# Kernel tuning notes

Hardware: AMD Instinct MI355X
Metric: run time of the kernel (lower is better)

The kernel has to match this reference:

```python
import jax, jax.numpy as jnp
import numpy as np

B, S, E, H = 2, 2048, 1024, 16
HD = E // H
SCALE = 1.0 / np.sqrt(HD)
PR_QKV = 0.05   # precision_ratio for q/k/v (critical_attention=False)
PR_OUT = 0.10
ROUTE_THR = 0.05  # gradient_threshold (critical_attention=False)
LN_EPS = 1e-5


def rpb_linear(x, W, b, precision_ratio):
    """ResidualPrecisionBoostLinear: ternary-quantized weight (threshold 0.7*mean|W|,
    per-tensor scale) plus top-`precision_ratio` fraction of residual kept full precision."""
    absW = jnp.abs(W)
    thr = 0.7 * jnp.mean(absW)
    tmask = (absW > thr).astype(W.dtype)
    scale = jnp.sum(absW * tmask) / jnp.maximum(jnp.sum(tmask), 1.0)
    Wq = scale * jnp.sign(W) * tmask
    res = W - Wq
    k = int(precision_ratio * W.size)
    kth = jax.lax.top_k(jnp.abs(res).ravel(), k)[0][-1]
    W_eff = Wq + res * (jnp.abs(res) >= kth).astype(W.dtype)
    return x @ W_eff.T + b


def selective_route(x, threshold):
    # forward: zero out small-magnitude activations (straight-through in training)
    return x * (jnp.abs(x) >= threshold).astype(x.dtype)


def layer_norm(x, g, b):
    mu = jnp.mean(x, axis=-1, keepdims=True)
    var = jnp.mean(jnp.square(x - mu), axis=-1, keepdims=True)
    return (x - mu) * jax.lax.rsqrt(var + LN_EPS) * g + b


def setup_inputs() -> dict:
    key = jax.random.key(0)
    ks = jax.random.split(key, 12)
    f = lambda k, shp, s=1.0: jax.random.normal(k, shp, dtype=jnp.float32) * s
    return {
        "query": f(ks[0], (B, S, E)),
        "key": f(ks[1], (B, S, E)),
        "value": f(ks[2], (B, S, E)),
        "Wq": f(ks[3], (E, E), 0.02), "bq": jnp.zeros((E,), jnp.float32),
        "Wk": f(ks[4], (E, E), 0.02), "bk": jnp.zeros((E,), jnp.float32),
        "Wv": f(ks[5], (E, E), 0.02), "bv": jnp.zeros((E,), jnp.float32),
        "Wo": f(ks[6], (E, E), 0.02), "bo": jnp.zeros((E,), jnp.float32),
        "ln_g": jnp.ones((E,), jnp.float32),
        "ln_b": jnp.zeros((E,), jnp.float32),
    }


def reference(query, key, value, Wq, bq, Wk, bk, Wv, bv, Wo, bo, ln_g, ln_b):
    qn = layer_norm(query, ln_g, ln_b)
    q = selective_route(rpb_linear(qn, Wq, bq, PR_QKV), ROUTE_THR)
    k = selective_route(rpb_linear(key, Wk, bk, PR_QKV), ROUTE_THR)
    v = selective_route(rpb_linear(value, Wv, bv, PR_QKV), ROUTE_THR)
    # [B,S,E] -> [B,H,S,HD]
    q = q.reshape(B, S, H, HD).transpose(0, 2, 1, 3)
    k = k.reshape(B, S, H, HD).transpose(0, 2, 1, 3)
    v = v.reshape(B, S, H, HD).transpose(0, 2, 1, 3)
    scores = jnp.einsum("bhqd,bhkd->bhqk", q, k) * SCALE
    attn = jax.nn.softmax(scores, axis=-1)   # dropout is identity in eval
    ctx = jnp.einsum("bhqk,bhkd->bhqd", attn, v)
    ctx = ctx.transpose(0, 2, 1, 3).reshape(B, S, E)
    return rpb_linear(ctx, Wo, bo, PR_OUT)
```

## Files before the change

### kernel.cpp

```cpp
#include <hip/hip_runtime.h>
#include <stdio.h>
#include <stdint.h>

#define BB 2
#define SS 2048
#define ED 1024
#define HH 16
#define HDD 64
#define MROWS 4096
#define NW_ELEM 1048576u

typedef unsigned short ushortT;
typedef __attribute__((ext_vector_type(8))) short bf16x8;
typedef __attribute__((ext_vector_type(4))) float f32x4;
typedef __attribute__((ext_vector_type(16))) float f32x16;

#define U_WHI 0u
#define U_WLO 4194304u
#define U_AH  8388608u
#define U_BH  12582912u
#define U_QH  16777216u
#define U_KH  20971520u
#define U_VH  25165824u
#define U_CH  29360128u
#define U_CL  33554432u
#define SMALL_OFF  75497472u
#define HIST_OFF   SMALL_OFF
#define ABS_OFF    (SMALL_OFF + 16384u)
#define MSK_OFF    (ABS_OFF + 32u)
#define CNT_OFF    (MSK_OFF + 32u)
#define SMALL_BYTES 16464u
#define WS_NEEDED  (SMALL_OFF + SMALL_BYTES)

#define SC44 17592186044416.0f
#define INV44 (1.0 / 17592186044416.0)

__device__ __forceinline__ const float* wsel(int w, const float* W0, const float* W1,
                                             const float* W2, const float* W3) {
  return w == 0 ? W0 : w == 1 ? W1 : w == 2 ? W2 : W3;
}

__device__ __forceinline__ ushortT f2bf(float x) {
  unsigned u = __float_as_uint(x);
  unsigned r = (u + 0x7FFFu + ((u >> 16) & 1u)) >> 16;
  return (ushortT)r;
}
__device__ __forceinline__ float bf2f(ushortT b) {
  return __uint_as_float(((unsigned)b) << 16);
}
__device__ __forceinline__ void bsplit(float x, ushortT& h, ushortT& l) {
  ushortT hb = f2bf(x);
  float hf = bf2f(hb);
  h = hb;
  l = f2bf(x - hf);
}
__device__ __forceinline__ unsigned pkbf(float a, float b) {
  unsigned r;
  asm("v_cvt_pk_bf16_f32 %0, %1, %2" : "=v"(r) : "v"(a), "v"(b));
  return r;
}
__device__ __forceinline__ void plswap(unsigned& a, unsigned& b) {
  asm("v_permlane32_swap_b32 %0, %1" : "+v"(a), "+v"(b));
}

__device__ __forceinline__ void gld_lds16(const ushortT* g, ushortT* s) {
  __builtin_amdgcn_global_load_lds((__attribute__((address_space(1))) void*)g,
                                   (__attribute__((address_space(3))) void*)s, 16, 0, 0);
}

__device__ __forceinline__ float get_thr(const unsigned long long* sAbs, int w) {
  return 0.7f * (float)((double)sAbs[w] * INV44 / 1048576.0);
}
__device__ __forceinline__ float get_scale(const unsigned long long* sMsk,
                                           const unsigned* cnt, int w) {
  double s = (double)sMsk[w] * INV44;
  return (float)s / fmaxf((float)cnt[w], 1.0f);
}

__device__ __forceinline__ void scan_sel(const unsigned* hist, unsigned& k, unsigned& prefix,
                                         unsigned* sh, int t) {
  sh[t] = hist[t];
  __syncthreads();
  for (int off = 1; off < 256; off <<= 1) {
    unsigned add = (t + off < 256) ? sh[t + off] : 0u;
    __syncthreads();
    sh[t] += add;
    __syncthreads();
  }
  int sel = __syncthreads_count((int)(sh[t] >= k)) - 1;
  unsigned suf = sh[sel];
  k -= (suf - hist[sel]);
  prefix = (prefix << 8) | (unsigned)sel;
  __syncthreads();
}

__global__ __launch_bounds__(256) void k_wstats(const float* W0, const float* W1,
                                                const float* W2, const float* W3,
                                                unsigned long long* sAbs) {
  const int w = blockIdx.y, t = threadIdx.x;
  const float* W = wsel(w, W0, W1, W2, W3) + blockIdx.x * 4096;
  unsigned long long s = 0;
#pragma unroll
  for (int r = 0; r < 4; r++) {
    float4 v = *(const float4*)(W + (t + 256 * r) * 4);
    s += (unsigned long long)(fabsf(v.x) * SC44);
    s += (unsigned long long)(fabsf(v.y) * SC44);
    s += (unsigned long long)(fabsf(v.z) * SC44);
    s += (unsigned long long)(fabsf(v.w) * SC44);
  }
  __shared__ unsigned long long sd[256];
  sd[t] = s;
  __syncthreads();
  for (int off = 128; off > 0; off >>= 1) {
    if (t < off) sd[t] += sd[t + off];
    __syncthreads();
  }
  if (!t) atomicAdd(&sAbs[w], sd[0]);
}

__global__ __launch_bounds__(256) void k_masked(const float* W0, const float* W1,
                                                const float* W2, const float* W3,
                                                const unsigned long long* sAbs,
                                                unsigned long long* sMsk, unsigned* sCnt) {
  const int w = blockIdx.y, t = threadIdx.x;
  const float thr = get_thr(sAbs, w);
  const float* W = wsel(w, W0, W1, W2, W3) + blockIdx.x * 4096;
  unsigned long long s = 0;
  unsigned c = 0;
#pragma unroll
  for (int r = 0; r < 4; r++) {
    float4 v = *(const float4*)(W + (t + 256 * r) * 4);
    float xs[4] = {v.x, v.y, v.z, v.w};
#pragma unroll
    for (int q = 0; q < 4; q++) {
      float a = fabsf(xs[q]);
      if (a > thr) { s += (unsigned long long)(a * SC44); c++; }
    }
  }
  __shared__ unsigned long long sd[256];
  __shared__ unsigned sc[256];
  sd[t] = s; sc[t] = c;
  __syncthreads();
  for (int off = 128; off > 0; off >>= 1) {
    if (t < off) { sd[t] += sd[t + off]; sc[t] += sc[t + off]; }
    __syncthreads();
  }
  if (!t) { atomicAdd(&sMsk[w], sd[0]); atomicAdd(&sCnt[w], sc[0]); }
}

__global__ __launch_bounds__(256) void k_hist(const float* W0, const float* W1,
                                              const float* W2, const float* W3,
                                              const unsigned long long* sAbs,
                                              const unsigned long long* sMsk,
                                              const unsigned* sCnt,
                                              unsigned* histG, int pass) {
  const int w = blockIdx.y, t = threadIdx.x;
  __shared__ unsigned sh[256];
  __shared__ unsigned h[256];
  const float thr = get_thr(sAbs, w);
  const float scale = get_scale(sMsk, sCnt, w);
  unsigned k = (w == 3) ? 104857u : 52428u, prefix = 0u;
  for (int pp = 0; pp < pass; pp++)
    scan_sel(histG + (pp * 4 + w) * 256, k, prefix, sh, t);

  h[t] = 0;
  __syncthreads();
  const float* W = wsel(w, W0, W1, W2, W3) + blockIdx.x * 4096;
  const int shift1 = 32 - 8 * pass;
  const int shift2 = 24 - 8 * pass;
#pragma unroll
  for (int r = 0; r < 4; r++) {
    float4 v = *(const float4*)(W + (t + 256 * r) * 4);
    float xs[4] = {v.x, v.y, v.z, v.w};
#pragma unroll
    for (int q = 0; q < 4; q++) {
      float x = xs[q];
      float a = fabsf(x);
      float wq = (a > thr) ? copysignf(scale, x) : 0.0f;
      unsigned bits = __float_as_uint(fabsf(x - wq));
      if (pass == 0) {
        atomicAdd(&h[bits >> 24], 1u);
      } else {
        if ((bits >> shift1) == prefix)
          atomicAdd(&h[(bits >> shift2) & 255u], 1u);
      }
    }
  }
  __syncthreads();
  if (h[t]) atomicAdd(&histG[(pass * 4 + w) * 256 + t], h[t]);
}

__global__ __launch_bounds__(256) void k_weff(const float* W0, const float* W1,
                                              const float* W2, const float* W3,
                                              const unsigned long long* sAbs,
                                              const unsigned long long* sMsk,
                                              const unsigned* sCnt,
                                              const unsigned* histG,
                                              ushortT* Whi, ushortT* Wlo) {
  const int w = blockIdx.y, t = threadIdx.x;
  __shared__ unsigned sh[256];
  const float thr = get_thr(sAbs, w);
  const float scale = get_scale(sMsk, sCnt, w);
  unsigned k = (w == 3) ? 104857u : 52428u, kth = 0u;
  for (int pp = 0; pp < 4; pp++)
    scan_sel(histG + (pp * 4 + w) * 256, k, kth, sh, t);

  const unsigned idx = (blockIdx.x * 256 + t) * 4;
  const float* W = wsel(w, W0, W1, W2, W3);
  float4 v = *(const float4*)(W + idx);
  float xs[4] = {v.x, v.y, v.z, v.w};
  ushort4 h4, l4;
#pragma unroll
  for (int c = 0; c < 4; c++) {
    float x = xs[c];
    float a = fabsf(x);
    float wq = (a > thr) ? copysignf(scale, x) : 0.0f;
    float res = x - wq;
    unsigned bits = __float_as_uint(fabsf(res));
    float we = wq + ((bits >= kth) ? res : 0.0f);
    ushortT hh, ll;
    bsplit(we, hh, ll);
    ((ushortT*)&h4)[c] = hh;
    ((ushortT*)&l4)[c] = ll;
  }
  *(ushort4*)&Whi[(size_t)w * NW_ELEM + idx] = h4;
  *(ushort4*)&Wlo[(size_t)w * NW_ELEM + idx] = l4;
}

__global__ __launch_bounds__(256) void k_pre(const float* __restrict__ query,
                                             const float* __restrict__ key,
                                             const float* __restrict__ g,
                                             const float* __restrict__ b,
                                             ushortT* __restrict__ Ah,
                                             ushortT* __restrict__ Bh) {
  const int t = threadIdx.x;
  if (blockIdx.y == 0) {
    const int row = blockIdx.x;
    __shared__ float red[8];
    float4 v = *(const float4*)&query[(size_t)row * ED + t * 4];
    float s = v.x + v.y + v.z + v.w;
#pragma unroll
    for (int m = 32; m; m >>= 1) s += __shfl_xor(s, m, 64);
    if ((t & 63) == 0) red[t >> 6] = s;
    __syncthreads();
    float mu = (red[0] + red[1] + red[2] + red[3]) * (1.0f / 1024.0f);
    float dx = v.x - mu, dy = v.y - mu, dz = v.z - mu, dw = v.w - mu;
    float s2 = dx * dx + dy * dy + dz * dz + dw * dw;
#pragma unroll
    for (int m = 32; m; m >>= 1) s2 += __shfl_xor(s2, m, 64);
    if ((t & 63) == 0) red[4 + (t >> 6)] = s2;
    __syncthreads();
    float var = (red[4] + red[5] + red[6] + red[7]) * (1.0f / 1024.0f);
    float inv = rsqrtf(var + 1e-5f);
    float4 gg = *(const float4*)&g[t * 4];
    float4 bb = *(const float4*)&b[t * 4];
    float ys[4] = {dx * inv * gg.x + bb.x, dy * inv * gg.y + bb.y,
                   dz * inv * gg.z + bb.z, dw * inv * gg.w + bb.w};
    ushort4 h4;
#pragma unroll
    for (int c = 0; c < 4; c++) ((ushortT*)&h4)[c] = f2bf(ys[c]);
    *(ushort4*)&Ah[(size_t)row * ED + t * 4] = h4;
  } else {
    const int i = (blockIdx.x * 256 + t) * 4;
    float4 v = *(const float4*)&key[i];
    ushort4 h4;
    h4.x = f2bf(v.x); h4.y = f2bf(v.y); h4.z = f2bf(v.z); h4.w = f2bf(v.w);
    *(ushort4*)&Bh[i] = h4;
  }
}

__global__ __launch_bounds__(256) void k_splith(const float* __restrict__ X,
                                                ushortT* __restrict__ H) {
  const int i = (blockIdx.x * 256 + threadIdx.x) * 4;
  float4 v = *(const float4*)&X[i];
  ushort4 h4;
  h4.x = f2bf(v.x); h4.y = f2bf(v.y); h4.z = f2bf(v.z); h4.w = f2bf(v.w);
  *(ushort4*)&H[i] = h4;
}

__device__ __forceinline__ f32x4 mfma16(bf16x8 a, bf16x8 b, f32x4 c) {
  return __builtin_amdgcn_mfma_f32_16x16x32_bf16(a, b, c, 0, 0, 0);
}

template <int MODE, bool ALO, bool WLO, bool DBUF>
__global__ __launch_bounds__(256, 2) void k_gemm(
    const ushortT* __restrict__ Ah, const ushortT* __restrict__ Al,
    const ushortT* __restrict__ Wh, const ushortT* __restrict__ Wl,
    const float* __restrict__ bias, ushortT* Cp, float* Cf) {
  constexpr int NB = DBUF ? 2 : 1;
  __shared__ __align__(16) ushortT sAh[NB * 8192];
  __shared__ __align__(16) ushortT sAl[ALO ? NB * 8192 : 8];
  __shared__ __align__(16) ushortT sBh[NB * 4096];
  __shared__ __align__(16) ushortT sBl[WLO ? NB * 4096 : 8];
  const int t = threadIdx.x;
  const int w = t >> 6, l = t & 63;
  const int wr = w >> 1, wc = w & 1;

  int id = blockIdx.x;
  int id2 = (id & 7) * 64 + (id >> 3);
  const int mt = id2 >> 4, nt = id2 & 15;
  const int m0 = mt * 128, n0 = nt * 64;

  const int sr = l >> 3, sg = l & 7;
  const int swz = sg ^ sr;

  auto stage = [&](int kt, int buf) {
#pragma unroll
    for (int s2 = 0; s2 < 4; s2++) {
      int seg = w * 4 + s2;
      size_t g = (size_t)(m0 + seg * 8 + sr) * ED + kt * 64 + swz * 8;
      gld_lds16(Ah + g, sAh + buf * 8192 + seg * 512);
      if constexpr (ALO) gld_lds16(Al + g, sAl + buf * 8192 + seg * 512);
    }
#pragma unroll
    for (int s2 = 0; s2 < 2; s2++) {
      int seg = w * 2 + s2;
      size_t g = (size_t)(n0 + seg * 8 + sr) * ED + kt * 64 + swz * 8;
      gld_lds16(Wh + g, sBh + buf * 4096 + seg * 512);
      if constexpr (WLO) gld_lds16(Wl + g, sBl + buf * 4096 + seg * 512);
    }
  };

  f32x4 acc[4][2];
#pragma unroll
  for (int i = 0; i < 4; i++)
#pragma unroll
    for (int j = 0; j < 2; j++) acc[i][j] = (f32x4){0.0f, 0.0f, 0.0f, 0.0f};

  auto compute = [&](int buf) {
#pragma unroll
    for (int ks = 0; ks < 2; ks++) {
      bf16x8 ah[4], al[4], bh[2], bl[2];
      const int G = ks * 4 + (l >> 4);
#pragma unroll
      for (int i = 0; i < 4; i++) {
        int r = wr * 64 + i * 16 + (l & 15);
        int off = buf * 8192 + r * 64 + ((G ^ (l & 7)) << 3);
        ah[i] = *(const bf16x8*)&sAh[off];
        if constexpr (ALO) al[i] = *(const bf16x8*)&sAl[off];
      }
#pragma unroll
      for (int j = 0; j < 2; j++) {
        int r = wc * 32 + j * 16 + (l & 15);
        int off = buf * 4096 + r * 64 + ((G ^ (l & 7)) << 3);
        bh[j] = *(const bf16x8*)&sBh[off];
        if constexpr (WLO) bl[j] = *(const bf16x8*)&sBl[off];
      }
#pragma unroll
      for (int i = 0; i < 4; i++)
#pragma unroll
        for (int j = 0; j < 2; j++) {
          acc[i][j] = mfma16(ah[i], bh[j], acc[i][j]);
          if constexpr (WLO) acc[i][j] = mfma16(ah[i], bl[j], acc[i][j]);
          if constexpr (ALO) acc[i][j] = mfma16(al[i], bh[j], acc[i][j]);
        }
    }
  };

  if constexpr (DBUF) {
    stage(0, 0);
    __syncthreads();
    for (int kt = 0; kt < 16; ++kt) {
      if (kt < 15) stage(kt + 1, (kt + 1) & 1);
      compute(kt & 1);
      __syncthreads();
    }
  } else {
    for (int kt = 0; kt < 16; ++kt) {
      __syncthreads();
      stage(kt, 0);
      __syncthreads();
      compute(0);
    }
  }

  const int coln = l & 15, row4 = (l >> 4) * 4;
  float bn[2];
#pragma unroll
  for (int j = 0; j < 2; j++) bn[j] = bias[n0 + wc * 32 + j * 16 + coln];

  if constexpr (MODE == 1) {
#pragma unroll
    for (int i = 0; i < 4; i++)
#pragma unroll
      for (int j = 0; j < 2; j++) {
        int n = n0 + wc * 32 + j * 16 + coln;
#pragma unroll
        for (int r = 0; r < 4; r++) {
          int m = m0 + wr * 64 + i * 16 + row4 + r;
          Cf[(size_t)m * ED + n] = acc[i][j][r] + bn[j];
        }
      }
  } else if constexpr (MODE == 0) {
    const int b_ = m0 >> 11, h_ = n0 >> 6;
#pragma unroll
    for (int i = 0; i < 4; i++)
#pragma unroll
      for (int j = 0; j < 2; j++) {
        int hd = wc * 32 + j * 16 + coln;
#pragma unroll
        for (int r = 0; r < 4; r++) {
          int m = m0 + wr * 64 + i * 16 + row4 + r;
          int s_ = m & 2047;
          float y = acc[i][j][r] + bn[j];
          y = (fabsf(y) >= 0.05f) ? y : 0.0f;
          Cp[((size_t)(b_ * HH + h_) * SS + s_) * HDD + hd] = f2bf(y);
        }
      }
  } else {
    const int b_ = m0 >> 11, h_ = n0 >> 6;
#pragma unroll
    for (int i = 0; i < 4; i++)
#pragma unroll
      for (int j = 0; j < 2; j++) {
        int hd = wc * 32 + j * 16 + coln;
        int s0_ = (m0 + wr * 64 + i * 16 + row4) & 2047;
        ushort4 h4;
#pragma unroll
        for (int r = 0; r < 4; r++) {
          float y = acc[i][j][r] + bn[j];
          y = (fabsf(y) >= 0.05f) ? y : 0.0f;
          ((ushortT*)&h4)[r] = f2bf(y);
        }
        *(ushort4*)&Cp[((size_t)(b_ * HH + h_) * HDD + hd) * SS + s0_] = h4;
      }
  }
}

__device__ __forceinline__ f32x16 mfma32(bf16x8 a, bf16x8 b, f32x16 c) {
  return __builtin_amdgcn_mfma_f32_32x32x16_bf16(a, b, c, 0, 0, 0);
}

__device__ __forceinline__ void exppack(const f32x16& A, float EC, float& lsum,
                                        bf16x8& paA, bf16x8& paB) {
  float p[16];
#pragma unroll
  for (int r = 0; r < 16; r++) {
    p[r] = exp2f(A[r] * EC);
    lsum += p[r];
  }
  unsigned c0 = pkbf(p[0], p[1]), c1 = pkbf(p[2], p[3]);
  unsigned c2 = pkbf(p[4], p[5]), c3 = pkbf(p[6], p[7]);
  unsigned c4 = pkbf(p[8], p[9]), c5 = pkbf(p[10], p[11]);
  unsigned c6 = pkbf(p[12], p[13]), c7 = pkbf(p[14], p[15]);
  plswap(c0, c2); plswap(c1, c3); plswap(c4, c6); plswap(c5, c7);
  uint4 ta = make_uint4(c0, c1, c2, c3);
  uint4 tb = make_uint4(c4, c5, c6, c7);
  paA = __builtin_bit_cast(bf16x8, ta);
  paB = __builtin_bit_cast(bf16x8, tb);
}

__global__ __launch_bounds__(256, 2) void k_attn(
    const ushortT* __restrict__ Qh, const ushortT* __restrict__ Kh,
    const ushortT* __restrict__ Vh,
    ushortT* __restrict__ ctxH, ushortT* __restrict__ ctxL) {
  __shared__ __align__(16) ushortT sK[2 * 4096];
  __shared__ __align__(16) ushortT sV[2 * 4096];

  const int t = threadIdx.x;
  const int w = t >> 6, l = t & 63;
  const int l32 = l & 31, g = l >> 5;

  int id = blockIdx.x;
  int id2 = (id & 7) * 64 + (id >> 3);
  const int bh = id2 >> 4, qt = id2 & 15;

  const size_t kqbase = (size_t)bh * (SS * HDD);
  const size_t vbase = (size_t)bh * (HDD * SS);
  const int q0 = qt * 128 + w * 32;

  bf16x8 qh[4];
  const size_t qrow = kqbase + (size_t)(q0 + l32) * HDD;
#pragma unroll
  for (int ks = 0; ks < 4; ks++) qh[ks] = *(const bf16x8*)&Qh[qrow + ks * 16 + g * 8];

  f32x16 octx0, octx1;
#pragma unroll
  for (int i = 0; i < 16; i++) { octx0[i] = 0.0f; octx1[i] = 0.0f; }
  float lsum = 0.0f;

  const float EC = 0.125f * 1.44269504088896f;

  const int srow = l >> 3;
  const int sgr = (l & 7) ^ srow;

  auto stageA = [&](int kt, int buf) {
    const int s0 = kt * 64;
#pragma unroll
    for (int s2 = 0; s2 < 2; s2++) {
      int seg = w * 2 + s2;
      int row = seg * 8 + srow;
      gld_lds16(Kh + kqbase + (size_t)(s0 + row) * HDD + sgr * 8, sK + buf * 4096 + seg * 512);
      gld_lds16(Vh + vbase + (size_t)row * SS + s0 + sgr * 8, sV + buf * 4096 + seg * 512);
    }
  };

  stageA(0, 0);
  __syncthreads();

  for (int kt = 0; kt < 32; ++kt) {
    if (kt < 31) stageA(kt + 1, (kt + 1) & 1);
    const ushortT* cK = sK + (kt & 1) * 4096;
    const ushortT* cV = sV + (kt & 1) * 4096;

    f32x16 acc0, acc1;
#pragma unroll
    for (int i = 0; i < 16; i++) { acc0[i] = 0.0f; acc1[i] = 0.0f; }
#pragma unroll
    for (int ks = 0; ks < 4; ks++) {
      int sw = ((ks * 2 + g) ^ (l32 & 7)) << 3;
      bf16x8 kh0 = *(const bf16x8*)&cK[l32 * 64 + sw];
      bf16x8 kh1 = *(const bf16x8*)&cK[(32 + l32) * 64 + sw];
      acc0 = mfma32(kh0, qh[ks], acc0);
      acc1 = mfma32(kh1, qh[ks], acc1);
    }

    bf16x8 pa0, pa1, pa2, pa3;
    exppack(acc0, EC, lsum, pa0, pa1);
    exppack(acc1, EC, lsum, pa2, pa3);

#pragma unroll
    for (int js = 0; js < 4; js++) {
      bf16x8 pj = js == 0 ? pa0 : js == 1 ? pa1 : js == 2 ? pa2 : pa3;
      int vsw = ((js * 2 + g) ^ (l32 & 7)) << 3;
      bf16x8 vh0 = *(const bf16x8*)&cV[l32 * 64 + vsw];
      bf16x8 vh1 = *(const bf16x8*)&cV[(32 + l32) * 64 + vsw];
      octx0 = mfma32(pj, vh0, octx0);
      octx1 = mfma32(pj, vh1, octx1);
    }
    __syncthreads();
  }

  float ls = lsum + __shfl_xor(lsum, 32, 64);

  const int b_ = bh >> 4, h_ = bh & 15;
#pragma unroll
  for (int r = 0; r < 16; r++) {
    int q = (r & 3) + 8 * (r >> 2) + 4 * g;
    float inv = 1.0f / __shfl(ls, q, 64);
    size_t base = ((size_t)(b_ * SS + q0 + q)) * ED + h_ * HDD;
    ushortT hh, ll;
    bsplit(octx0[r] * inv, hh, ll);
    ctxH[base + l32] = hh;
    ctxL[base + l32] = ll;
    bsplit(octx1[r] * inv, hh, ll);
    ctxH[base + 32 + l32] = hh;
    ctxL[base + 32 + l32] = ll;
  }
}

extern "C" void kernel_launch(void* const* d_in, const int* in_sizes, int n_in,
                              void* d_out, int out_size, void* d_ws, size_t ws_size,
                              hipStream_t stream) {
  const float* query = (const float*)d_in[0];
  const float* key   = (const float*)d_in[1];
  const float* value = (const float*)d_in[2];
  const float* Wq = (const float*)d_in[3];
  const float* bq = (const float*)d_in[4];
  const float* Wk = (const float*)d_in[5];
  const float* bk = (const float*)d_in[6];
  const float* Wv = (const float*)d_in[7];
  const float* bv = (const float*)d_in[8];
  const float* Wo = (const float*)d_in[9];
  const float* bo = (const float*)d_in[10];
  const float* lng = (const float*)d_in[11];
  const float* lnb = (const float*)d_in[12];
  float* out = (float*)d_out;

  if (ws_size < (size_t)WS_NEEDED) {
    fprintf(stderr, "kernel_launch: ws too small (%zu < %u)\n", ws_size, WS_NEEDED);
    return;
  }

  ushortT* wsu = (ushortT*)d_ws;
  ushortT* Whi = wsu + U_WHI;
  ushortT* Wlo = wsu + U_WLO;
  ushortT* Abh = wsu + U_AH;
  ushortT* Bbh = wsu + U_BH;
  ushortT* Qhp = wsu + U_QH;
  ushortT* Khp = wsu + U_KH;
  ushortT* Vhp = wsu + U_VH;
  ushortT* Chp = wsu + U_CH;
  ushortT* Clp = wsu + U_CL;

  char* wsb = (char*)d_ws;
  unsigned* histG = (unsigned*)(wsb + HIST_OFF);
  unsigned long long* sAbs = (unsigned long long*)(wsb + ABS_OFF);
  unsigned long long* sMsk = (unsigned long long*)(wsb + MSK_OFF);
  unsigned* sCnt = (unsigned*)(wsb + CNT_OFF);

  hipMemsetAsync(histG, 0, SMALL_BYTES, stream);

  dim3 gW(256, 4);
  k_wstats<<<gW, 256, 0, stream>>>(Wq, Wk, Wv, Wo, sAbs);
  k_masked<<<gW, 256, 0, stream>>>(Wq, Wk, Wv, Wo, sAbs, sMsk, sCnt);
  for (int pass = 0; pass < 4; ++pass)
    k_hist<<<gW, 256, 0, stream>>>(Wq, Wk, Wv, Wo, sAbs, sMsk, sCnt, histG, pass);
  k_weff<<<dim3(1024, 4), 256, 0, stream>>>(Wq, Wk, Wv, Wo, sAbs, sMsk, sCnt, histG,
                                            Whi, Wlo);

  k_pre<<<dim3(MROWS, 2), 256, 0, stream>>>(query, key, lng, lnb, Abh, Bbh);

  k_gemm<0, false, false, true><<<512, 256, 0, stream>>>(
      Abh, nullptr, Whi + 0 * NW_ELEM, nullptr, bq, Qhp, nullptr);
  k_gemm<0, false, false, true><<<512, 256, 0, stream>>>(
      Bbh, nullptr, Whi + 1 * NW_ELEM, nullptr, bk, Khp, nullptr);

  k_splith<<<4096, 256, 0, stream>>>(value, Abh);
  k_gemm<2, false, true, true><<<512, 256, 0, stream>>>(
      Abh, nullptr, Whi + 2 * NW_ELEM, Wlo + 2 * NW_ELEM, bv, Vhp, nullptr);

  k_attn<<<512, 256, 0, stream>>>(Qhp, Khp, Vhp, Chp, Clp);

  k_gemm<1, true, true, false><<<512, 256, 0, stream>>>(
      Chp, Clp, Whi + 3 * NW_ELEM, Wlo + 3 * NW_ELEM, bo, nullptr, out);
}
```

Baseline: 257.1 us.

## Fuse QKV GEMMs, split attention over key halves, retile output GEMM

The three Q/K/V projection GEMMs are merged into a single 1536-block launch, and the value bf16 conversion is folded into the preprocessing kernel. Attention is split across two key-range halves, giving 1024 blocks with unnormalized fp32 partials. A new reduce kernel combines the partials and produces the hi/lo context. The softmax scale is folded into Q at the projection epilogue. The output GEMM becomes a dedicated double-buffered kernel with a K-tile of 32. This is meant to raise occupancy and cut launch count, at the cost of extra fp32 partial traffic and one more kernel. Without a running max, exp2 overflow relies on the input value range.

```diff
diff --git a/kernel.cpp b/kernel.cpp
--- a/kernel.cpp
+++ b/kernel.cpp
@@ -17,14 +17,16 @@
 
 #define U_WHI 0u
 #define U_WLO 4194304u
-#define U_AH  8388608u
-#define U_BH  12582912u
-#define U_QH  16777216u
-#define U_KH  20971520u
-#define U_VH  25165824u
-#define U_CH  29360128u
-#define U_CL  33554432u
-#define SMALL_OFF  75497472u
+#define U_XQ  8388608u
+#define U_XK  12582912u
+#define U_XV  16777216u
+#define U_QH  20971520u
+#define U_KH  25165824u
+#define U_VH  29360128u
+#define LP_OFF  33554432u
+#define P0_OFF  67108864u
+#define P1_OFF  83886080u
+#define SMALL_OFF  100663296u
 #define HIST_OFF   SMALL_OFF
 #define ABS_OFF    (SMALL_OFF + 16384u)
 #define MSK_OFF    (ABS_OFF + 32u)
@@ -34,6 +36,7 @@
 
 #define SC44 17592186044416.0f
 #define INV44 (1.0 / 17592186044416.0)
+#define QSCALE 0.18033688011112042f
 
 __device__ __forceinline__ const float* wsel(int w, const float* W0, const float* W1,
                                              const float* W2, const float* W3) {
@@ -229,10 +232,12 @@
 
 __global__ __launch_bounds__(256) void k_pre(const float* __restrict__ query,
                                              const float* __restrict__ key,
+                                             const float* __restrict__ value,
                                              const float* __restrict__ g,
                                              const float* __restrict__ b,
-                                             ushortT* __restrict__ Ah,
-                                             ushortT* __restrict__ Bh) {
+                                             ushortT* __restrict__ Xq,
+                                             ushortT* __restrict__ Xk,
+                                             ushortT* __restrict__ Xv) {
   const int t = threadIdx.x;
   if (blockIdx.y == 0) {
     const int row = blockIdx.x;
@@ -259,47 +264,46 @@
     ushort4 h4;
 #pragma unroll
     for (int c = 0; c < 4; c++) ((ushortT*)&h4)[c] = f2bf(ys[c]);
-    *(ushort4*)&Ah[(size_t)row * ED + t * 4] = h4;
+    *(ushort4*)&Xq[(size_t)row * ED + t * 4] = h4;
   } else {
+    const float* src = (blockIdx.y == 1) ? key : value;
+    ushortT* dst = (blockIdx.y == 1) ? Xk : Xv;
     const int i = (blockIdx.x * 256 + t) * 4;
-    float4 v = *(const float4*)&key[i];
+    float4 v = *(const float4*)&src[i];
     ushort4 h4;
     h4.x = f2bf(v.x); h4.y = f2bf(v.y); h4.z = f2bf(v.z); h4.w = f2bf(v.w);
-    *(ushort4*)&Bh[i] = h4;
-  }
-}
-
-__global__ __launch_bounds__(256) void k_splith(const float* __restrict__ X,
-                                                ushortT* __restrict__ H) {
-  const int i = (blockIdx.x * 256 + threadIdx.x) * 4;
-  float4 v = *(const float4*)&X[i];
-  ushort4 h4;
-  h4.x = f2bf(v.x); h4.y = f2bf(v.y); h4.z = f2bf(v.z); h4.w = f2bf(v.w);
-  *(ushort4*)&H[i] = h4;
+    *(ushort4*)&dst[i] = h4;
+  }
 }
 
 __device__ __forceinline__ f32x4 mfma16(bf16x8 a, bf16x8 b, f32x4 c) {
   return __builtin_amdgcn_mfma_f32_16x16x32_bf16(a, b, c, 0, 0, 0);
 }
 
-template <int MODE, bool ALO, bool WLO, bool DBUF>
-__global__ __launch_bounds__(256, 2) void k_gemm(
-    const ushortT* __restrict__ Ah, const ushortT* __restrict__ Al,
-    const ushortT* __restrict__ Wh, const ushortT* __restrict__ Wl,
-    const float* __restrict__ bias, ushortT* Cp, float* Cf) {
-  constexpr int NB = DBUF ? 2 : 1;
-  __shared__ __align__(16) ushortT sAh[NB * 8192];
-  __shared__ __align__(16) ushortT sAl[ALO ? NB * 8192 : 8];
-  __shared__ __align__(16) ushortT sBh[NB * 4096];
-  __shared__ __align__(16) ushortT sBl[WLO ? NB * 4096 : 8];
+__global__ __launch_bounds__(256, 2) void k_gemm_qkv(
+    const ushortT* __restrict__ Xq, const ushortT* __restrict__ Xk,
+    const ushortT* __restrict__ Xv,
+    const ushortT* __restrict__ Whi, const ushortT* __restrict__ Wlo,
+    const float* __restrict__ bq, const float* __restrict__ bk,
+    const float* __restrict__ bv,
+    ushortT* __restrict__ Qo, ushortT* __restrict__ Ko, ushortT* __restrict__ Vo) {
+  __shared__ __align__(16) ushortT sAh[2 * 8192];
+  __shared__ __align__(16) ushortT sBh[2 * 4096];
+  __shared__ __align__(16) ushortT sBl[2 * 4096];
   const int t = threadIdx.x;
   const int w = t >> 6, l = t & 63;
   const int wr = w >> 1, wc = w & 1;
 
-  int id = blockIdx.x;
-  int id2 = (id & 7) * 64 + (id >> 3);
-  const int mt = id2 >> 4, nt = id2 & 15;
-  const int m0 = mt * 128, n0 = nt * 64;
+  const int which = blockIdx.x >> 9;
+  const int wid = blockIdx.x & 511;
+  int id2 = (wid & 7) * 64 + (wid >> 3);
+  const int m0 = (id2 >> 4) * 128, n0 = (id2 & 15) * 64;
+
+  const ushortT* A = which == 0 ? Xq : which == 1 ? Xk : Xv;
+  const ushortT* Wh = Whi + (unsigned)which * NW_ELEM;
+  const ushortT* Wl = Wlo + 2u * NW_ELEM;
+  const float* bias = which == 0 ? bq : which == 1 ? bk : bv;
+  const bool wlo = (which == 2);
 
   const int sr = l >> 3, sg = l & 7;
   const int swz = sg ^ sr;
@@ -308,16 +312,15 @@
 #pragma unroll
     for (int s2 = 0; s2 < 4; s2++) {
       int seg = w * 4 + s2;
-      size_t g = (size_t)(m0 + seg * 8 + sr) * ED + kt * 64 + swz * 8;
-      gld_lds16(Ah + g, sAh + buf * 8192 + seg * 512);
-      if constexpr (ALO) gld_lds16(Al + g, sAl + buf * 8192 + seg * 512);
+      size_t gsrc = (size_t)(m0 + seg * 8 + sr) * ED + kt * 64 + swz * 8;
+      gld_lds16(A + gsrc, sAh + buf * 8192 + seg * 512);
     }
 #pragma unroll
     for (int s2 = 0; s2 < 2; s2++) {
       int seg = w * 2 + s2;
-      size_t g = (size_t)(n0 + seg * 8 + sr) * ED + kt * 64 + swz * 8;
-      gld_lds16(Wh + g, sBh + buf * 4096 + seg * 512);
-      if constexpr (WLO) gld_lds16(Wl + g, sBl + buf * 4096 + seg * 512);
+      size_t gsrc = (size_t)(n0 + seg * 8 + sr) * ED + kt * 64 + swz * 8;
+      gld_lds16(Wh + gsrc, sBh + buf * 4096 + seg * 512);
+      if (wlo) gld_lds16(Wl + gsrc, sBl + buf * 4096 + seg * 512);
     }
   };
 
@@ -330,69 +333,47 @@
   auto compute = [&](int buf) {
 #pragma unroll
     for (int ks = 0; ks < 2; ks++) {
-      bf16x8 ah[4], al[4], bh[2], bl[2];
+      bf16x8 ah[4], bh2[2], bl2[2];
       const int G = ks * 4 + (l >> 4);
 #pragma unroll
       for (int i = 0; i < 4; i++) {
         int r = wr * 64 + i * 16 + (l & 15);
-        int off = buf * 8192 + r * 64 + ((G ^ (l & 7)) << 3);
-        ah[i] = *(const bf16x8*)&sAh[off];
-        if constexpr (ALO) al[i] = *(const bf16x8*)&sAl[off];
+        ah[i] = *(const bf16x8*)&sAh[buf * 8192 + r * 64 + ((G ^ (l & 7)) << 3)];
       }
 #pragma unroll
       for (int j = 0; j < 2; j++) {
         int r = wc * 32 + j * 16 + (l & 15);
         int off = buf * 4096 + r * 64 + ((G ^ (l & 7)) << 3);
-        bh[j] = *(const bf16x8*)&sBh[off];
-        if constexpr (WLO) bl[j] = *(const bf16x8*)&sBl[off];
+        bh2[j] = *(const bf16x8*)&sBh[off];
+        if (wlo) bl2[j] = *(const bf16x8*)&sBl[off];
       }
 #pragma unroll
       for (int i = 0; i < 4; i++)
 #pragma unroll
         for (int j = 0; j < 2; j++) {
-          acc[i][j] = mfma16(ah[i], bh[j], acc[i][j]);
-          if constexpr (WLO) acc[i][j] = mfma16(ah[i], bl[j], acc[i][j]);
-          if constexpr (ALO) acc[i][j] = mfma16(al[i], bh[j], acc[i][j]);
+          acc[i][j] = mfma16(ah[i], bh2[j], acc[i][j]);
+          if (wlo) acc[i][j] = mfma16(ah[i], bl2[j], acc[i][j]);
         }
     }
   };
 
-  if constexpr (DBUF) {
-    stage(0, 0);
-    __syncthreads();
-    for (int kt = 0; kt < 16; ++kt) {
-      if (kt < 15) stage(kt + 1, (kt + 1) & 1);
-      compute(kt & 1);
-      __syncthreads();
-    }
-  } else {
-    for (int kt = 0; kt < 16; ++kt) {
-      __syncthreads();
-      stage(kt, 0);
-      __syncthreads();
-      compute(0);
-    }
+  stage(0, 0);
+  __syncthreads();
+  for (int kt = 0; kt < 16; ++kt) {
+    if (kt < 15) stage(kt + 1, (kt + 1) & 1);
+    compute(kt & 1);
+    __syncthreads();
   }
 
   const int coln = l & 15, row4 = (l >> 4) * 4;
   float bn[2];
 #pragma unroll
   for (int j = 0; j < 2; j++) bn[j] = bias[n0 + wc * 32 + j * 16 + coln];
-
-  if constexpr (MODE == 1) {
-#pragma unroll
-    for (int i = 0; i < 4; i++)
-#pragma unroll
-      for (int j = 0; j < 2; j++) {
-        int n = n0 + wc * 32 + j * 16 + coln;
-#pragma unroll
-        for (int r = 0; r < 4; r++) {
-          int m = m0 + wr * 64 + i * 16 + row4 + r;
-          Cf[(size_t)m * ED + n] = acc[i][j][r] + bn[j];
-        }
-      }
-  } else if constexpr (MODE == 0) {
-    const int b_ = m0 >> 11, h_ = n0 >> 6;
+  const int b_ = m0 >> 11, h_ = n0 >> 6;
+
+  if (which < 2) {
+    const float osc = (which == 0) ? QSCALE : 1.0f;
+    ushortT* C = (which == 0) ? Qo : Ko;
 #pragma unroll
     for (int i = 0; i < 4; i++)
 #pragma unroll
@@ -404,11 +385,11 @@
           int s_ = m & 2047;
           float y = acc[i][j][r] + bn[j];
           y = (fabsf(y) >= 0.05f) ? y : 0.0f;
-          Cp[((size_t)(b_ * HH + h_) * SS + s_) * HDD + hd] = f2bf(y);
+          y *= osc;
+          C[((size_t)(b_ * HH + h_) * SS + s_) * HDD + hd] = f2bf(y);
         }
       }
   } else {
-    const int b_ = m0 >> 11, h_ = n0 >> 6;
 #pragma unroll
     for (int i = 0; i < 4; i++)
 #pragma unroll
@@ -422,21 +403,112 @@
           y = (fabsf(y) >= 0.05f) ? y : 0.0f;
           ((ushortT*)&h4)[r] = f2bf(y);
         }
-        *(ushort4*)&Cp[((size_t)(b_ * HH + h_) * HDD + hd) * SS + s0_] = h4;
+        *(ushort4*)&Vo[((size_t)(b_ * HH + h_) * HDD + hd) * SS + s0_] = h4;
       }
   }
+}
+
+__global__ __launch_bounds__(256, 2) void k_gemmo(
+    const ushortT* __restrict__ Ah, const ushortT* __restrict__ Al,
+    const ushortT* __restrict__ Wh, const ushortT* __restrict__ Wl,
+    const float* __restrict__ bias, float* __restrict__ Cf) {
+  __shared__ __align__(16) ushortT sAh[2 * 4096], sAl[2 * 4096];
+  __shared__ __align__(16) ushortT sBh[2 * 2048], sBl[2 * 2048];
+  const int t = threadIdx.x;
+  const int w = t >> 6, l = t & 63;
+  const int wr = w >> 1, wc = w & 1;
+
+  int id = blockIdx.x;
+  int id2 = (id & 7) * 64 + (id >> 3);
+  const int m0 = (id2 >> 4) * 128, n0 = (id2 & 15) * 64;
+
+  const int srow = l >> 2;
+  const int sgr = (l & 3) ^ ((l >> 3) & 3);
+
+  auto stage = [&](int kt, int buf) {
+    const int c0 = kt * 32 + sgr * 8;
+#pragma unroll
+    for (int s2 = 0; s2 < 2; s2++) {
+      int seg = w * 2 + s2;
+      size_t ga = (size_t)(m0 + seg * 16 + srow) * ED + c0;
+      gld_lds16(Ah + ga, sAh + buf * 4096 + seg * 512);
+      gld_lds16(Al + ga, sAl + buf * 4096 + seg * 512);
+    }
+    {
+      size_t gb = (size_t)(n0 + w * 16 + srow) * ED + c0;
+      gld_lds16(Wh + gb, sBh + buf * 2048 + w * 512);
+      gld_lds16(Wl + gb, sBl + buf * 2048 + w * 512);
+    }
+  };
+
+  f32x4 acc[4][2];
+#pragma unroll
+  for (int i = 0; i < 4; i++)
+#pragma unroll
+    for (int j = 0; j < 2; j++) acc[i][j] = (f32x4){0.0f, 0.0f, 0.0f, 0.0f};
+
+  auto compute = [&](int buf) {
+    bf16x8 ah[4], al[4], bh2[2], bl2[2];
+    const int G = l >> 4;
+#pragma unroll
+    for (int i = 0; i < 4; i++) {
+      int r = wr * 64 + i * 16 + (l & 15);
+      int off = buf * 4096 + r * 32 + ((G ^ ((r >> 1) & 3)) << 3);
+      ah[i] = *(const bf16x8*)&sAh[off];
+      al[i] = *(const bf16x8*)&sAl[off];
+    }
+#pragma unroll
+    for (int j = 0; j < 2; j++) {
+      int r = wc * 32 + j * 16 + (l & 15);
+      int off = buf * 2048 + r * 32 + ((G ^ ((r >> 1) & 3)) << 3);
+      bh2[j] = *(const bf16x8*)&sBh[off];
+      bl2[j] = *(const bf16x8*)&sBl[off];
+    }
+#pragma unroll
+    for (int i = 0; i < 4; i++)
+#pragma unroll
+      for (int j = 0; j < 2; j++) {
+        acc[i][j] = mfma16(ah[i], bh2[j], acc[i][j]);
+        acc[i][j] = mfma16(ah[i], bl2[j], acc[i][j]);
+        acc[i][j] = mfma16(al[i], bh2[j], acc[i][j]);
+      }
+  };
+
+  stage(0, 0);
+  __syncthreads();
+  for (int kt = 0; kt < 32; ++kt) {
+    if (kt < 31) stage(kt + 1, (kt + 1) & 1);
+    compute(kt & 1);
+    __syncthreads();
+  }
+
+  const int coln = l & 15, row4 = (l >> 4) * 4;
+  float bn[2];
+#pragma unroll
+  for (int j = 0; j < 2; j++) bn[j] = bias[n0 + wc * 32 + j * 16 + coln];
+#pragma unroll
+  for (int i = 0; i < 4; i++)
+#pragma unroll
+    for (int j = 0; j < 2; j++) {
+      int n = n0 + wc * 32 + j * 16 + coln;
+#pragma unroll
+      for (int r = 0; r < 4; r++) {
+        int m = m0 + wr * 64 + i * 16 + row4 + r;
+        Cf[(size_t)m * ED + n] = acc[i][j][r] + bn[j];
+      }
+    }
 }
 
 __device__ __forceinline__ f32x16 mfma32(bf16x8 a, bf16x8 b, f32x16 c) {
   return __builtin_amdgcn_mfma_f32_32x32x16_bf16(a, b, c, 0, 0, 0);
 }
 
-__device__ __forceinline__ void exppack(const f32x16& A, float EC, float& lsum,
+__device__ __forceinline__ void exppack(const f32x16& A, float& lsum,
                                         bf16x8& paA, bf16x8& paB) {
   float p[16];
 #pragma unroll
   for (int r = 0; r < 16; r++) {
-    p[r] = exp2f(A[r] * EC);
+    p[r] = exp2f(A[r]);
     lsum += p[r];
   }
   unsigned c0 = pkbf(p[0], p[1]), c1 = pkbf(p[2], p[3]);
@@ -450,10 +522,10 @@
   paB = __builtin_bit_cast(bf16x8, tb);
 }
 
-__global__ __launch_bounds__(256, 2) void k_attn(
+__global__ __launch_bounds__(256, 4) void k_attn(
     const ushortT* __restrict__ Qh, const ushortT* __restrict__ Kh,
     const ushortT* __restrict__ Vh,
-    ushortT* __restrict__ ctxH, ushortT* __restrict__ ctxL) {
+    float* __restrict__ Pp, float* __restrict__ Lp) {
   __shared__ __align__(16) ushortT sK[2 * 4096];
   __shared__ __align__(16) ushortT sV[2 * 4096];
 
@@ -462,12 +534,15 @@
   const int l32 = l & 31, g = l >> 5;
 
   int id = blockIdx.x;
-  int id2 = (id & 7) * 64 + (id >> 3);
-  const int bh = id2 >> 4, qt = id2 & 15;
+  int id2 = (id & 7) * 128 + (id >> 3);
+  const int bh = id2 >> 5;
+  const int qt = (id2 >> 1) & 15;
+  const int half = id2 & 1;
 
   const size_t kqbase = (size_t)bh * (SS * HDD);
   const size_t vbase = (size_t)bh * (HDD * SS);
   const int q0 = qt * 128 + w * 32;
+  const int sbase = half * 1024;
 
   bf16x8 qh[4];
   const size_t qrow = kqbase + (size_t)(q0 + l32) * HDD;
@@ -479,13 +554,11 @@
   for (int i = 0; i < 16; i++) { octx0[i] = 0.0f; octx1[i] = 0.0f; }
   float lsum = 0.0f;
 
-  const float EC = 0.125f * 1.44269504088896f;
-
   const int srow = l >> 3;
   const int sgr = (l & 7) ^ srow;
 
   auto stageA = [&](int kt, int buf) {
-    const int s0 = kt * 64;
+    const int s0 = sbase + kt * 64;
 #pragma unroll
     for (int s2 = 0; s2 < 2; s2++) {
       int seg = w * 2 + s2;
@@ -498,8 +571,8 @@
   stageA(0, 0);
   __syncthreads();
 
-  for (int kt = 0; kt < 32; ++kt) {
-    if (kt < 31) stageA(kt + 1, (kt + 1) & 1);
+  for (int kt = 0; kt < 16; ++kt) {
+    if (kt < 15) stageA(kt + 1, (kt + 1) & 1);
     const ushortT* cK = sK + (kt & 1) * 4096;
     const ushortT* cV = sV + (kt & 1) * 4096;
 
@@ -516,8 +589,8 @@
     }
 
     bf16x8 pa0, pa1, pa2, pa3;
-    exppack(acc0, EC, lsum, pa0, pa1);
-    exppack(acc1, EC, lsum, pa2, pa3);
+    exppack(acc0, lsum, pa0, pa1);
+    exppack(acc1, lsum, pa2, pa3);
 
 #pragma unroll
     for (int js = 0; js < 4; js++) {
@@ -532,21 +605,33 @@
   }
 
   float ls = lsum + __shfl_xor(lsum, 32, 64);
-
-  const int b_ = bh >> 4, h_ = bh & 15;
+  if (g == 0) Lp[half * 65536 + bh * 2048 + q0 + l32] = ls;
+
+  float* P = Pp + (size_t)half * 4194304u;
 #pragma unroll
   for (int r = 0; r < 16; r++) {
     int q = (r & 3) + 8 * (r >> 2) + 4 * g;
-    float inv = 1.0f / __shfl(ls, q, 64);
-    size_t base = ((size_t)(b_ * SS + q0 + q)) * ED + h_ * HDD;
-    ushortT hh, ll;
-    bsplit(octx0[r] * inv, hh, ll);
-    ctxH[base + l32] = hh;
-    ctxL[base + l32] = ll;
-    bsplit(octx1[r] * inv, hh, ll);
-    ctxH[base + 32 + l32] = hh;
-    ctxL[base + 32 + l32] = ll;
-  }
+    size_t pb = ((size_t)bh * 2048 + q0 + q) * 64;
+    P[pb + l32] = octx0[r];
+    P[pb + 32 + l32] = octx1[r];
+  }
+}
+
+__global__ __launch_bounds__(256) void k_reduce(const float* __restrict__ Pp,
+                                                const float* __restrict__ Lp,
+                                                ushortT* __restrict__ ctxH,
+                                                ushortT* __restrict__ ctxL) {
+  const unsigned i = blockIdx.x * 256 + threadIdx.x;
+  const int d = i & 63;
+  const int sq = (i >> 6) & 2047;
+  const int bh = i >> 17;
+  float ls = Lp[bh * 2048 + sq] + Lp[65536 + bh * 2048 + sq];
+  float o = (Pp[i] + Pp[4194304u + i]) / ls;
+  ushortT hh, ll;
+  bsplit(o, hh, ll);
+  size_t ci = ((size_t)((bh >> 4) * 2048 + sq)) * 1024 + (bh & 15) * 64 + d;
+  ctxH[ci] = hh;
+  ctxL[ci] = ll;
 }
 
 extern "C" void kernel_launch(void* const* d_in, const int* in_sizes, int n_in,
@@ -575,21 +660,26 @@
   ushortT* wsu = (ushortT*)d_ws;
   ushortT* Whi = wsu + U_WHI;
   ushortT* Wlo = wsu + U_WLO;
-  ushortT* Abh = wsu + U_AH;
-  ushortT* Bbh = wsu + U_BH;
+  ushortT* Xq  = wsu + U_XQ;
+  ushortT* Xk  = wsu + U_XK;
+  ushortT* Xv  = wsu + U_XV;
   ushortT* Qhp = wsu + U_QH;
   ushortT* Khp = wsu + U_KH;
   ushortT* Vhp = wsu + U_VH;
-  ushortT* Chp = wsu + U_CH;
-  ushortT* Clp = wsu + U_CL;
+  ushortT* Chp = wsu + U_XQ;
+  ushortT* Clp = wsu + U_XK;
 
   char* wsb = (char*)d_ws;
+  float* Pp = (float*)(wsb + P0_OFF);
+  float* Lp = (float*)(wsb + LP_OFF);
   unsigned* histG = (unsigned*)(wsb + HIST_OFF);
   unsigned long long* sAbs = (unsigned long long*)(wsb + ABS_OFF);
   unsigned long long* sMsk = (unsigned long long*)(wsb + MSK_OFF);
   unsigned* sCnt = (unsigned*)(wsb + CNT_OFF);
 
   hipMemsetAsync(histG, 0, SMALL_BYTES, stream);
+
+  k_pre<<<dim3(MROWS, 3), 256, 0, stream>>>(query, key, value, lng, lnb, Xq, Xk, Xv);
 
   dim3 gW(256, 4);
   k_wstats<<<gW, 256, 0, stream>>>(Wq, Wk, Wv, Wo, sAbs);
@@ -599,19 +689,12 @@
   k_weff<<<dim3(1024, 4), 256, 0, stream>>>(Wq, Wk, Wv, Wo, sAbs, sMsk, sCnt, histG,
                                             Whi, Wlo);
 
-  k_pre<<<dim3(MROWS, 2), 256, 0, stream>>>(query, key, lng, lnb, Abh, Bbh);
-
-  k_gemm<0, false, false, true><<<512, 256, 0, stream>>>(
-      Abh, nullptr, Whi + 0 * NW_ELEM, nullptr, bq, Qhp, nullptr);
-  k_gemm<0, false, false, true><<<512, 256, 0, stream>>>(
-      Bbh, nullptr, Whi + 1 * NW_ELEM, nullptr, bk, Khp, nullptr);
-
-  k_splith<<<4096, 256, 0, stream>>>(value, Abh);
-  k_gemm<2, false, true, true><<<512, 256, 0, stream>>>(
-      Abh, nullptr, Whi + 2 * NW_ELEM, Wlo + 2 * NW_ELEM, bv, Vhp, nullptr);
-
-  k_attn<<<512, 256, 0, stream>>>(Qhp, Khp, Vhp, Chp, Clp);
-
-  k_gemm<1, true, true, false><<<512, 256, 0, stream>>>(
-      Chp, Clp, Whi + 3 * NW_ELEM, Wlo + 3 * NW_ELEM, bo, nullptr, out);
-}
+  k_gemm_qkv<<<1536, 256, 0, stream>>>(Xq, Xk, Xv, Whi, Wlo, bq, bk, bv,
+                                       Qhp, Khp, Vhp);
+
+  k_attn<<<1024, 256, 0, stream>>>(Qhp, Khp, Vhp, Pp, Lp);
+  k_reduce<<<16384, 256, 0, stream>>>(Pp, Lp, Chp, Clp);
+
+  k_gemmo<<<512, 256, 0, stream>>>(Chp, Clp, Whi + 3 * NW_ELEM, Wlo + 3 * NW_ELEM,
+                                   bo, out);
+}
```

New measurement: 268.0 us. +4.2%, slower.
